# Optimization experiments

Hardware: AMD Instinct MI355X
Metric: run time of the kernel (lower is better)

Reference implementation:

```python
import jax, jax.numpy as jnp
import numpy as np

N_NODES = 100000
N_EDGES = 1200000
D = 64
N_LAYERS = 3


def setup_inputs() -> dict:
    key = jax.random.key(0)
    k0, k1, k2, k3, k4 = jax.random.split(key, 5)
    x = jax.random.normal(k0, (N_NODES, D), dtype=jnp.float32)
    edge_index = jax.random.randint(k1, (2, N_EDGES), 0, N_NODES, dtype=jnp.int32)
    edge_weight = jax.random.uniform(k2, (N_EDGES,), dtype=jnp.float32)
    # stacked per-layer params: 3 layers of 64->64
    self_kernels = jax.random.normal(k3, (N_LAYERS, D, D), dtype=jnp.float32) * 0.1
    neighbor_kernels = jax.random.normal(k4, (N_LAYERS, D, D), dtype=jnp.float32) * 0.1
    biases = jnp.zeros((N_LAYERS, D), dtype=jnp.float32)
    return {"x": x, "edge_index": edge_index, "edge_weight": edge_weight,
            "self_kernels": self_kernels, "neighbor_kernels": neighbor_kernels,
            "biases": biases}


def _sage_layer(h, row, col, edge_weight, self_k, neigh_k, b):
    # gather source-node features per edge, weight them: [E, d]
    msg = h[col] * edge_weight[:, None]
    # sum-aggregate messages at target nodes: [N, d]
    agg = jax.ops.segment_sum(msg, row, num_segments=N_NODES)
    # concat=False -> self transform + neighbor transform added, then relu
    out = h @ self_k + agg @ neigh_k + b
    return jax.nn.relu(out)


def reference(x, edge_index, edge_weight, self_kernels, neighbor_kernels, biases):
    row, col = edge_index[0], edge_index[1]
    h = x
    for i in range(N_LAYERS):
        h = _sage_layer(h, row, col, edge_weight,
                        self_kernels[i], neighbor_kernels[i], biases[i])
    return h
```

## Files before the change

### kernel.cpp

```cpp
#include <hip/hip_runtime.h>

#define NN 100000
#define NE 1200000
#define DD 64
#define NTILES 3125
#define NBK 391
#define MLEN (NBK * 256)
#define EPB 4688
#define ECAP 768

typedef unsigned int uint32;
typedef unsigned char uint8;
typedef unsigned short ushort16;
typedef __attribute__((ext_vector_type(8))) short short8;
typedef __attribute__((ext_vector_type(16))) float f32x16;

__device__ __forceinline__ ushort16 f2bf(float x) {
    uint32 u = __float_as_uint(x);
    u += 0x7FFFu + ((u >> 16) & 1u);
    return (ushort16)(u >> 16);
}
__device__ __forceinline__ float bflo(uint32 u) { return __uint_as_float(u << 16); }
__device__ __forceinline__ float bfhi(uint32 u) { return __uint_as_float(u & 0xFFFF0000u); }
__device__ __forceinline__ uint32 pack2(float a, float b) {
    return (uint32)f2bf(a) | ((uint32)f2bf(b) << 16);
}

__device__ __forceinline__ void agg_lds(float* a, int ls, int le, uint32 flB,
                                        const uint2* __restrict__ esh,
                                        const char* __restrict__ ybase) {
    #pragma unroll 4
    for (int j = ls; j < le; j++) {
        uint2 ei = esh[j];
        float w = __uint_as_float(ei.y);
        uint4 yv = *(const uint4*)(ybase + (ei.x + flB));
        a[0] = fmaf(bflo(yv.x), w, a[0]);
        a[1] = fmaf(bfhi(yv.x), w, a[1]);
        a[2] = fmaf(bflo(yv.y), w, a[2]);
        a[3] = fmaf(bfhi(yv.y), w, a[3]);
        a[4] = fmaf(bflo(yv.z), w, a[4]);
        a[5] = fmaf(bfhi(yv.z), w, a[5]);
        a[6] = fmaf(bflo(yv.w), w, a[6]);
        a[7] = fmaf(bfhi(yv.w), w, a[7]);
    }
}

__device__ __forceinline__ void agg_glob(float* a, int s, int e, uint32 flB,
                                         const uint32* __restrict__ edges,
                                         const char* __restrict__ ybase) {
    for (int j = s; j < e; j++) {
        uint32 ed = edges[j];
        float w = (float)(ed & 32767u) * (1.0f / 32767.0f);
        uint4 yv = *(const uint4*)(ybase + (((ed >> 15) << 7) + flB));
        a[0] = fmaf(bflo(yv.x), w, a[0]);
        a[1] = fmaf(bfhi(yv.x), w, a[1]);
        a[2] = fmaf(bflo(yv.y), w, a[2]);
        a[3] = fmaf(bfhi(yv.y), w, a[3]);
        a[4] = fmaf(bflo(yv.z), w, a[4]);
        a[5] = fmaf(bfhi(yv.z), w, a[5]);
        a[6] = fmaf(bflo(yv.w), w, a[6]);
        a[7] = fmaf(bfhi(yv.w), w, a[7]);
    }
}


__global__ __launch_bounds__(512)
void k_init(const int* __restrict__ row, int* __restrict__ M,
            const float* __restrict__ selfk, const float* __restrict__ neighk,
            short8* __restrict__ wpack, const float* __restrict__ x,
            ushort16* __restrict__ hs, ushort16* __restrict__ y,
            const float* __restrict__ biases) {
    if (blockIdx.x >= 262) {
        int lane  = threadIdx.x & 63;
        int wave  = threadIdx.x >> 6;
        int wid   = (blockIdx.x - 262) * 8 + wave;
        int mrow  = lane & 31;
        int khalf = lane >> 5;
        int t     = wid & 1;

        short8 Wf[2][4];
        #pragma unroll
        for (int g = 0; g < 2; g++) {
            const float* W = g ? neighk : selfk;
            #pragma unroll
            for (int s = 0; s < 4; s++) {
                int k0 = s * 16 + khalf * 8;
                short8 v;
                #pragma unroll
                for (int j = 0; j < 8; j++)
                    v[j] = (short)f2bf(W[(k0 + j) * 64 + t * 32 + mrow]);
                Wf[g][s] = v;
            }
        }
        float bval = biases[t * 32 + mrow];

        for (int tile = wid >> 1; tile < NTILES; tile += 1564) {
            int n0 = tile * 32;
            const float* hf = x + (n0 + mrow) * 64 + khalf * 8;
            short8 A[4];
            #pragma unroll
            for (int s = 0; s < 4; s++) {
                short8 a;
                #pragma unroll
                for (int j = 0; j < 8; j++) a[j] = (short)f2bf(hf[s * 16 + j]);
                A[s] = a;
            }

            f32x16 acc0, acc1;
            #pragma unroll
            for (int r = 0; r < 16; r++) { acc0[r] = 0.f; acc1[r] = 0.f; }

            #pragma unroll
            for (int s = 0; s < 4; s++) {
                acc0 = __builtin_amdgcn_mfma_f32_32x32x16_bf16(A[s], Wf[0][s], acc0, 0, 0, 0);
                acc1 = __builtin_amdgcn_mfma_f32_32x32x16_bf16(A[s], Wf[1][s], acc1, 0, 0, 0);
            }

            int colbase = t * 32 + mrow;
            #pragma unroll
            for (int r = 0; r < 16; r++) {
                int rw = (r & 3) + 8 * (r >> 2) + 4 * khalf;
                int nn = n0 + rw;
                hs[nn * DD + colbase] = f2bf(acc0[r] + bval);
                y [nn * DD + colbase] = f2bf(acc1[r]);
            }
        }
        return;
    }
    if (blockIdx.x >= 256) {
        int tid = (blockIdx.x - 256) * 512 + threadIdx.x;
        if (tid < 3 * 16 * 64) {
            int lane  = tid & 63;
            int frag  = (tid >> 6) & 15;
            int layer = tid >> 10;
            int g = frag >> 3;
            int t = (frag >> 2) & 1;
            int s = frag & 3;
            const float* W = (g ? neighk : selfk) + layer * 4096;
            int n = t * 32 + (lane & 31);
            int k0 = s * 16 + (lane >> 5) * 8;
            short8 v;
            #pragma unroll
            for (int j = 0; j < 8; j++) v[j] = (short)f2bf(W[(k0 + j) * 64 + n]);
            wpack[tid] = v;
        }
        return;
    }
    __shared__ int bins[NBK];
    for (int i = threadIdx.x; i < NBK; i += 512) bins[i] = 0;
    __syncthreads();
    int start = blockIdx.x * EPB;
    int end = min(start + EPB, NE);
    for (int e = start + (int)threadIdx.x; e < end; e += 512)
        atomicAdd(&bins[row[e] >> 8], 1);
    __syncthreads();
    for (int i = threadIdx.x; i < NBK; i += 512)
        M[i * 256 + blockIdx.x] = bins[i];
}


__global__ void k_scan1(const int* __restrict__ in, int* __restrict__ outx,
                        int* __restrict__ partials) {
    __shared__ int tmp[256];
    int t = threadIdx.x;
    int i = blockIdx.x * 256 + t;
    int v = (i < MLEN) ? in[i] : 0;
    tmp[t] = v;
    __syncthreads();
    #pragma unroll
    for (int off = 1; off < 256; off <<= 1) {
        int add = (t >= off) ? tmp[t - off] : 0;
        __syncthreads();
        tmp[t] += add;
        __syncthreads();
    }
    if (i < MLEN) outx[i] = tmp[t] - v;
    if (t == 255) partials[blockIdx.x] = tmp[255];
}

__global__ __launch_bounds__(512)
void k_bscatter(const int* __restrict__ row, const int* __restrict__ col,
                const float* __restrict__ ew, const int* __restrict__ Mscan,
                const int* __restrict__ partials, int* __restrict__ partials2,
                uint32* __restrict__ colw, uint8* __restrict__ rowlo) {
    __shared__ int tmp[512];
    __shared__ int cur[NBK];
    int t = threadIdx.x;
    int v = (t < NBK) ? partials[t] : 0;
    tmp[t] = v;
    __syncthreads();
    #pragma unroll
    for (int off = 1; off < 512; off <<= 1) {
        int add = (t >= off) ? tmp[t - off] : 0;
        __syncthreads();
        tmp[t] += add;
        __syncthreads();
    }
    if (t < NBK) {
        int excl = tmp[t] - v;
        cur[t] = Mscan[t * 256 + blockIdx.x] + excl;
        if (blockIdx.x == 0) partials2[t] = excl;
    }
    __syncthreads();
    int start = blockIdx.x * EPB;
    int end = min(start + EPB, NE);
    for (int e = start + (int)threadIdx.x; e < end; e += 512) {
        int r = row[e];
        int wq = (int)(ew[e] * 32767.0f + 0.5f);
        wq = (wq > 32767) ? 32767 : wq;
        int p = atomicAdd(&cur[r >> 8], 1);
        colw[p]  = ((uint32)col[e] << 15) | (uint32)wq;
        rowlo[p] = (uint8)(r & 255);
    }
}

__global__ __launch_bounds__(256)
void k_build(const int* __restrict__ Mscan, const int* __restrict__ partials2,
             const uint32* __restrict__ colw, const uint8* __restrict__ rowlo,
             uint32* __restrict__ edges, int* __restrict__ offsets) {
    __shared__ int bins[256];
    __shared__ int tmp[256];
    __shared__ int cur[256];
    int b = blockIdx.x;
    int t = threadIdx.x;
    int bstart = Mscan[b * 256] + partials2[b];
    int bend   = (b == NBK - 1) ? NE : Mscan[(b + 1) * 256] + partials2[b + 1];
    bins[t] = 0;
    __syncthreads();
    for (int p = bstart + t; p < bend; p += 256)
        atomicAdd(&bins[rowlo[p]], 1);
    __syncthreads();
    int v = bins[t];
    tmp[t] = v;
    __syncthreads();
    #pragma unroll
    for (int off = 1; off < 256; off <<= 1) {
        int add = (t >= off) ? tmp[t - off] : 0;
        __syncthreads();
        tmp[t] += add;
        __syncthreads();
    }
    int base = bstart + (tmp[t] - v);
    cur[t] = base;
    int rowid = b * 256 + t;
    if (rowid < NN) offsets[rowid] = base;
    if (b == 0 && t == 0) offsets[NN] = NE;
    __syncthreads();
    for (int p = bstart + t; p < bend; p += 256) {
        uint32 cw = colw[p];
        int dst = atomicAdd(&cur[rowlo[p]], 1);
        edges[dst] = cw;
    }
}


__global__ __launch_bounds__(256)
void agg_gemm(const uint4* __restrict__ hs4, const uint4* __restrict__ y4,
              ushort16* __restrict__ hs_out, ushort16* __restrict__ y_out,
              const int* __restrict__ offsets, const uint32* __restrict__ edges,
              const short8* __restrict__ wpack, const float* __restrict__ bias) {
    __shared__ uint32 sh[32 * 36];
    __shared__ uint2 esh[ECAP];
    int lane = threadIdx.x & 63;
    int wave = threadIdx.x >> 6;
    int g  = lane >> 3;
    int fl = lane & 7;
    int n0 = blockIdx.x * 32;
    int lrow = wave * 8 + g;
    int n = n0 + lrow;

    int ebase = offsets[n0];
    int m = min(offsets[n0 + 32] - ebase, ECAP);
    for (int i = threadIdx.x; i < m; i += 256) {
        uint32 ed = edges[ebase + i];
        esh[i] = make_uint2((ed >> 15) << 7,
                            __float_as_uint((float)(ed & 32767u) * (1.0f / 32767.0f)));
    }
    int s = offsets[n];
    int e = offsets[n + 1];
    uint4 hv = hs4[n * 8 + fl];
    __syncthreads();

    float a[8] = {bflo(hv.x), bfhi(hv.x), bflo(hv.y), bfhi(hv.y),
                  bflo(hv.z), bfhi(hv.z), bflo(hv.w), bfhi(hv.w)};
    uint32 flB = (uint32)fl * 16u;
    const char* ybase = (const char*)y4;
    int ls = s - ebase, le = e - ebase;
    agg_lds(a, min(ls, ECAP), min(le, ECAP), flB, esh, ybase);
    if (le > ECAP)
        agg_glob(a, ebase + max(ls, ECAP), ebase + le, flB, edges, ybase);

    uint32* dstp = &sh[lrow * 36 + fl * 4];
    dstp[0] = pack2(fmaxf(a[0], 0.f), fmaxf(a[1], 0.f));
    dstp[1] = pack2(fmaxf(a[2], 0.f), fmaxf(a[3], 0.f));
    dstp[2] = pack2(fmaxf(a[4], 0.f), fmaxf(a[5], 0.f));
    dstp[3] = pack2(fmaxf(a[6], 0.f), fmaxf(a[7], 0.f));
    __syncthreads();

    int mrow  = lane & 31;
    int khalf = lane >> 5;
    int gsel  = wave >> 1;
    int t     = wave & 1;

    short8 Wf[4];
    #pragma unroll
    for (int ss = 0; ss < 4; ss++)
        Wf[ss] = wpack[(((gsel * 2 + t) * 4) + ss) * 64 + lane];

    short8 A[4];
    #pragma unroll
    for (int ss = 0; ss < 4; ss++)
        A[ss] = *(const short8*)&sh[mrow * 36 + ss * 8 + khalf * 4];

    f32x16 acc;
    #pragma unroll
    for (int r = 0; r < 16; r++) acc[r] = 0.f;
    #pragma unroll
    for (int ss = 0; ss < 4; ss++)
        acc = __builtin_amdgcn_mfma_f32_32x32x16_bf16(A[ss], Wf[ss], acc, 0, 0, 0);

    float bval = gsel ? 0.f : bias[t * 32 + mrow];
    ushort16* dst = gsel ? y_out : hs_out;
    int colbase = t * 32 + mrow;
    #pragma unroll
    for (int r = 0; r < 16; r++) {
        int rw = (r & 3) + 8 * (r >> 2) + 4 * khalf;
        dst[(n0 + rw) * DD + colbase] = f2bf(acc[r] + bval);
    }
}


__global__ __launch_bounds__(256)
void agg_final(const uint4* __restrict__ hs4, const uint4* __restrict__ y4,
               float4* __restrict__ out, const int* __restrict__ offsets,
               const uint32* __restrict__ edges) {
    __shared__ uint2 esh[ECAP];
    int lane = threadIdx.x & 63;
    int wave = threadIdx.x >> 6;
    int g  = lane >> 3;
    int fl = lane & 7;
    int n0 = blockIdx.x * 32;
    int n = n0 + wave * 8 + g;

    int ebase = offsets[n0];
    int m = min(offsets[n0 + 32] - ebase, ECAP);
    for (int i = threadIdx.x; i < m; i += 256) {
        uint32 ed = edges[ebase + i];
        esh[i] = make_uint2((ed >> 15) << 7,
                            __float_as_uint((float)(ed & 32767u) * (1.0f / 32767.0f)));
    }
    int s = offsets[n];
    int e = offsets[n + 1];
    uint4 hv = hs4[n * 8 + fl];
    __syncthreads();

    float a[8] = {bflo(hv.x), bfhi(hv.x), bflo(hv.y), bfhi(hv.y),
                  bflo(hv.z), bfhi(hv.z), bflo(hv.w), bfhi(hv.w)};
    uint32 flB = (uint32)fl * 16u;
    const char* ybase = (const char*)y4;
    int ls = s - ebase, le = e - ebase;
    agg_lds(a, min(ls, ECAP), min(le, ECAP), flB, esh, ybase);
    if (le > ECAP)
        agg_glob(a, ebase + max(ls, ECAP), ebase + le, flB, edges, ybase);

    out[n * 16 + fl * 2]     = make_float4(fmaxf(a[0], 0.f), fmaxf(a[1], 0.f),
                                           fmaxf(a[2], 0.f), fmaxf(a[3], 0.f));
    out[n * 16 + fl * 2 + 1] = make_float4(fmaxf(a[4], 0.f), fmaxf(a[5], 0.f),
                                           fmaxf(a[6], 0.f), fmaxf(a[7], 0.f));
}


extern "C" void kernel_launch(void* const* d_in, const int* in_sizes, int n_in,
                              void* d_out, int out_size, void* d_ws, size_t ws_size,
                              hipStream_t stream) {
    const float* x      = (const float*)d_in[0];
    const int*   ei     = (const int*)d_in[1];
    const float* ew     = (const float*)d_in[2];
    const float* selfk  = (const float*)d_in[3];
    const float* neighk = (const float*)d_in[4];
    const float* biases = (const float*)d_in[5];
    float* out = (float*)d_out;

    char* w = (char*)d_ws;
    ushort16* hsA   = (ushort16*)w; w += (size_t)NN * DD * sizeof(ushort16);
    ushort16* yA    = (ushort16*)w; w += (size_t)NN * DD * sizeof(ushort16);
    ushort16* hsB   = (ushort16*)w; w += (size_t)NN * DD * sizeof(ushort16);
    ushort16* yB    = (ushort16*)w; w += (size_t)NN * DD * sizeof(ushort16);
    uint32* edges   = (uint32*)w;   w += (size_t)NE * sizeof(uint32);
    uint32* colwB   = (uint32*)w;   w += (size_t)NE * sizeof(uint32);
    uint8*  rowlo   = (uint8*)w;    w += (size_t)NE * sizeof(uint8);
    w = (char*)(((size_t)w + 255) & ~(size_t)255);
    int*    M       = (int*)w;      w += (size_t)MLEN * sizeof(int);
    int*    Mscan   = (int*)w;      w += (size_t)MLEN * sizeof(int);
    int*    offsets = (int*)w;      w += (size_t)(NN + 1) * sizeof(int);
    int*    partials= (int*)w;      w += 512 * sizeof(int);
    int*    partials2=(int*)w;      w += 512 * sizeof(int);
    short8* wpack   = (short8*)w;   w += (size_t)3 * 16 * 64 * sizeof(short8);

    const int* row = ei;
    const int* col = ei + NE;

    k_init    <<<653, 512, 0, stream>>>(row, M, selfk, neighk, wpack,
                                        x, hsA, yA, biases);
    k_scan1   <<<NBK, 256, 0, stream>>>(M, Mscan, partials);
    k_bscatter<<<256, 512, 0, stream>>>(row, col, ew, Mscan, partials, partials2,
                                        colwB, rowlo);
    k_build   <<<NBK, 256, 0, stream>>>(Mscan, partials2, colwB, rowlo, edges, offsets);

    agg_gemm <<<NTILES, 256, 0, stream>>>((const uint4*)hsA, (const uint4*)yA,
                                          hsB, yB, offsets, edges,
                                          wpack + 1024, biases + 64);
    agg_gemm <<<NTILES, 256, 0, stream>>>((const uint4*)hsB, (const uint4*)yB,
                                          hsA, yA, offsets, edges,
                                          wpack + 2048, biases + 128);
    agg_final<<<NTILES, 256, 0, stream>>>((const uint4*)hsA, (const uint4*)yA,
                                          (float4*)out, offsets, edges);
}
```

Measured before the change: 231.9 us.

## Balance edge aggregation across rows with LDS atomics and segment partitioning

Replaces per-row CSR aggregation, where each 8-lane group walked its own node's edge list, with an edge-balanced scheme. The block's edges are split evenly across the 32 row groups, each edge is tagged with its local row via binary search, and per-run partial sums are flushed to an LDS fp32 accumulator with atomics. The aim is to remove load imbalance from skewed node degrees, at the cost of extra LDS traffic and atomics. It also raises the LDS edge cache capacity and vectorizes the fp32 input loads in the init GEMM.

```diff
diff --git a/kernel.cpp b/kernel.cpp
--- a/kernel.cpp
+++ b/kernel.cpp
@@ -7,7 +7,7 @@
 #define NBK 391
 #define MLEN (NBK * 256)
 #define EPB 4688
-#define ECAP 768
+#define ECAP 1024
 
 typedef unsigned int uint32;
 typedef unsigned char uint8;
@@ -24,43 +24,6 @@
 __device__ __forceinline__ float bfhi(uint32 u) { return __uint_as_float(u & 0xFFFF0000u); }
 __device__ __forceinline__ uint32 pack2(float a, float b) {
     return (uint32)f2bf(a) | ((uint32)f2bf(b) << 16);
-}
-
-__device__ __forceinline__ void agg_lds(float* a, int ls, int le, uint32 flB,
-                                        const uint2* __restrict__ esh,
-                                        const char* __restrict__ ybase) {
-    #pragma unroll 4
-    for (int j = ls; j < le; j++) {
-        uint2 ei = esh[j];
-        float w = __uint_as_float(ei.y);
-        uint4 yv = *(const uint4*)(ybase + (ei.x + flB));
-        a[0] = fmaf(bflo(yv.x), w, a[0]);
-        a[1] = fmaf(bfhi(yv.x), w, a[1]);
-        a[2] = fmaf(bflo(yv.y), w, a[2]);
-        a[3] = fmaf(bfhi(yv.y), w, a[3]);
-        a[4] = fmaf(bflo(yv.z), w, a[4]);
-        a[5] = fmaf(bfhi(yv.z), w, a[5]);
-        a[6] = fmaf(bflo(yv.w), w, a[6]);
-        a[7] = fmaf(bfhi(yv.w), w, a[7]);
-    }
-}
-
-__device__ __forceinline__ void agg_glob(float* a, int s, int e, uint32 flB,
-                                         const uint32* __restrict__ edges,
-                                         const char* __restrict__ ybase) {
-    for (int j = s; j < e; j++) {
-        uint32 ed = edges[j];
-        float w = (float)(ed & 32767u) * (1.0f / 32767.0f);
-        uint4 yv = *(const uint4*)(ybase + (((ed >> 15) << 7) + flB));
-        a[0] = fmaf(bflo(yv.x), w, a[0]);
-        a[1] = fmaf(bfhi(yv.x), w, a[1]);
-        a[2] = fmaf(bflo(yv.y), w, a[2]);
-        a[3] = fmaf(bfhi(yv.y), w, a[3]);
-        a[4] = fmaf(bflo(yv.z), w, a[4]);
-        a[5] = fmaf(bfhi(yv.z), w, a[5]);
-        a[6] = fmaf(bflo(yv.w), w, a[6]);
-        a[7] = fmaf(bfhi(yv.w), w, a[7]);
-    }
 }
 
 
@@ -96,13 +59,18 @@
 
         for (int tile = wid >> 1; tile < NTILES; tile += 1564) {
             int n0 = tile * 32;
-            const float* hf = x + (n0 + mrow) * 64 + khalf * 8;
+            const float4* hf4 = (const float4*)(x + (size_t)(n0 + mrow) * 64)
+                                + khalf * 2;
             short8 A[4];
             #pragma unroll
             for (int s = 0; s < 4; s++) {
+                float4 q0 = hf4[s * 4];
+                float4 q1 = hf4[s * 4 + 1];
                 short8 a;
-                #pragma unroll
-                for (int j = 0; j < 8; j++) a[j] = (short)f2bf(hf[s * 16 + j]);
+                a[0] = (short)f2bf(q0.x); a[1] = (short)f2bf(q0.y);
+                a[2] = (short)f2bf(q0.z); a[3] = (short)f2bf(q0.w);
+                a[4] = (short)f2bf(q1.x); a[5] = (short)f2bf(q1.y);
+                a[6] = (short)f2bf(q1.z); a[7] = (short)f2bf(q1.w);
                 A[s] = a;
             }
 
@@ -259,42 +227,114 @@
               ushort16* __restrict__ hs_out, ushort16* __restrict__ y_out,
               const int* __restrict__ offsets, const uint32* __restrict__ edges,
               const short8* __restrict__ wpack, const float* __restrict__ bias) {
-    __shared__ uint32 sh[32 * 36];
-    __shared__ uint2 esh[ECAP];
-    int lane = threadIdx.x & 63;
-    int wave = threadIdx.x >> 6;
+    __shared__ __align__(16) uint32 ubuf[ECAP * 2];
+    __shared__ float sacc[32 * 65];
+    __shared__ int loff[33];
+    uint2* esh = (uint2*)ubuf;
+    int tid  = threadIdx.x;
+    int lane = tid & 63;
+    int wave = tid >> 6;
     int g  = lane >> 3;
     int fl = lane & 7;
     int n0 = blockIdx.x * 32;
     int lrow = wave * 8 + g;
     int n = n0 + lrow;
 
-    int ebase = offsets[n0];
-    int m = min(offsets[n0 + 32] - ebase, ECAP);
-    for (int i = threadIdx.x; i < m; i += 256) {
+    if (tid < 33) loff[tid] = offsets[n0 + tid];
+    uint4 hv = hs4[n * 8 + fl];
+    {
+        float* ap = &sacc[lrow * 65 + fl * 8];
+        ap[0] = bflo(hv.x); ap[1] = bfhi(hv.x);
+        ap[2] = bflo(hv.y); ap[3] = bfhi(hv.y);
+        ap[4] = bflo(hv.z); ap[5] = bfhi(hv.z);
+        ap[6] = bflo(hv.w); ap[7] = bfhi(hv.w);
+    }
+    __syncthreads();
+
+    int ebase = loff[0];
+    int m  = loff[32] - ebase;
+    int mm = min(m, ECAP);
+    for (int i = tid; i < mm; i += 256) {
         uint32 ed = edges[ebase + i];
-        esh[i] = make_uint2((ed >> 15) << 7,
+        int gi = ebase + i;
+        int lo = 0, hi = 32;
+        #pragma unroll
+        for (int st = 0; st < 5; st++) {
+            int mid = (lo + hi) >> 1;
+            if (loff[mid] <= gi) lo = mid; else hi = mid;
+        }
+        esh[i] = make_uint2(((ed >> 15) << 7) | (uint32)lo,
                             __float_as_uint((float)(ed & 32767u) * (1.0f / 32767.0f)));
     }
-    int s = offsets[n];
-    int e = offsets[n + 1];
-    uint4 hv = hs4[n * 8 + fl];
-    __syncthreads();
-
-    float a[8] = {bflo(hv.x), bfhi(hv.x), bflo(hv.y), bfhi(hv.y),
-                  bflo(hv.z), bfhi(hv.z), bflo(hv.w), bfhi(hv.w)};
+    __syncthreads();
+
     uint32 flB = (uint32)fl * 16u;
     const char* ybase = (const char*)y4;
-    int ls = s - ebase, le = e - ebase;
-    agg_lds(a, min(ls, ECAP), min(le, ECAP), flB, esh, ybase);
-    if (le > ECAP)
-        agg_glob(a, ebase + max(ls, ECAP), ebase + le, flB, edges, ybase);
-
-    uint32* dstp = &sh[lrow * 36 + fl * 4];
-    dstp[0] = pack2(fmaxf(a[0], 0.f), fmaxf(a[1], 0.f));
-    dstp[1] = pack2(fmaxf(a[2], 0.f), fmaxf(a[3], 0.f));
-    dstp[2] = pack2(fmaxf(a[4], 0.f), fmaxf(a[5], 0.f));
-    dstp[3] = pack2(fmaxf(a[6], 0.f), fmaxf(a[7], 0.f));
+    int chunk = (mm + 31) >> 5;
+    int j0 = lrow * chunk;
+    int j1 = min(j0 + chunk, mm);
+    float r0=0.f,r1=0.f,r2=0.f,r3=0.f,r4=0.f,r5=0.f,r6=0.f,r7=0.f;
+    int curr = -1;
+    #pragma unroll 2
+    for (int j = j0; j < j1; j++) {
+        uint2 e = esh[j];
+        int r = (int)(e.x & 31u);
+        float w = __uint_as_float(e.y);
+        uint4 yv = *(const uint4*)(ybase + ((e.x & 0xFFFFFF80u) + flB));
+        if (r != curr) {
+            if (curr >= 0) {
+                float* p = &sacc[curr * 65 + fl * 8];
+                atomicAdd(p+0, r0); atomicAdd(p+1, r1);
+                atomicAdd(p+2, r2); atomicAdd(p+3, r3);
+                atomicAdd(p+4, r4); atomicAdd(p+5, r5);
+                atomicAdd(p+6, r6); atomicAdd(p+7, r7);
+            }
+            r0=r1=r2=r3=r4=r5=r6=r7=0.f;
+            curr = r;
+        }
+        r0 = fmaf(bflo(yv.x), w, r0);
+        r1 = fmaf(bfhi(yv.x), w, r1);
+        r2 = fmaf(bflo(yv.y), w, r2);
+        r3 = fmaf(bfhi(yv.y), w, r3);
+        r4 = fmaf(bflo(yv.z), w, r4);
+        r5 = fmaf(bfhi(yv.z), w, r5);
+        r6 = fmaf(bflo(yv.w), w, r6);
+        r7 = fmaf(bfhi(yv.w), w, r7);
+    }
+    if (curr >= 0) {
+        float* p = &sacc[curr * 65 + fl * 8];
+        atomicAdd(p+0, r0); atomicAdd(p+1, r1);
+        atomicAdd(p+2, r2); atomicAdd(p+3, r3);
+        atomicAdd(p+4, r4); atomicAdd(p+5, r5);
+        atomicAdd(p+6, r6); atomicAdd(p+7, r7);
+    }
+    for (int i = ECAP + lrow; i < m; i += 32) {
+        uint32 ed = edges[ebase + i];
+        int gi = ebase + i;
+        int lo = 0, hi = 32;
+        for (int st = 0; st < 5; st++) {
+            int mid = (lo + hi) >> 1;
+            if (loff[mid] <= gi) lo = mid; else hi = mid;
+        }
+        float w = (float)(ed & 32767u) * (1.0f / 32767.0f);
+        uint4 yv = *(const uint4*)(ybase + (((ed >> 15) << 7) + flB));
+        float* p = &sacc[lo * 65 + fl * 8];
+        atomicAdd(p+0, bflo(yv.x)*w); atomicAdd(p+1, bfhi(yv.x)*w);
+        atomicAdd(p+2, bflo(yv.y)*w); atomicAdd(p+3, bfhi(yv.y)*w);
+        atomicAdd(p+4, bflo(yv.z)*w); atomicAdd(p+5, bfhi(yv.z)*w);
+        atomicAdd(p+6, bflo(yv.w)*w); atomicAdd(p+7, bfhi(yv.w)*w);
+    }
+    __syncthreads();
+
+    uint32* sh = ubuf;
+    {
+        float* q = &sacc[lrow * 65 + fl * 8];
+        uint32* dstp = &sh[lrow * 36 + fl * 4];
+        dstp[0] = pack2(fmaxf(q[0], 0.f), fmaxf(q[1], 0.f));
+        dstp[1] = pack2(fmaxf(q[2], 0.f), fmaxf(q[3], 0.f));
+        dstp[2] = pack2(fmaxf(q[4], 0.f), fmaxf(q[5], 0.f));
+        dstp[3] = pack2(fmaxf(q[6], 0.f), fmaxf(q[7], 0.f));
+    }
     __syncthreads();
 
     int mrow  = lane & 31;
@@ -334,39 +374,110 @@
 void agg_final(const uint4* __restrict__ hs4, const uint4* __restrict__ y4,
                float4* __restrict__ out, const int* __restrict__ offsets,
                const uint32* __restrict__ edges) {
-    __shared__ uint2 esh[ECAP];
-    int lane = threadIdx.x & 63;
-    int wave = threadIdx.x >> 6;
+    __shared__ __align__(16) uint32 ubuf[ECAP * 2];
+    __shared__ float sacc[32 * 65];
+    __shared__ int loff[33];
+    uint2* esh = (uint2*)ubuf;
+    int tid  = threadIdx.x;
+    int lane = tid & 63;
+    int wave = tid >> 6;
     int g  = lane >> 3;
     int fl = lane & 7;
     int n0 = blockIdx.x * 32;
-    int n = n0 + wave * 8 + g;
-
-    int ebase = offsets[n0];
-    int m = min(offsets[n0 + 32] - ebase, ECAP);
-    for (int i = threadIdx.x; i < m; i += 256) {
+    int lrow = wave * 8 + g;
+    int n = n0 + lrow;
+
+    if (tid < 33) loff[tid] = offsets[n0 + tid];
+    uint4 hv = hs4[n * 8 + fl];
+    {
+        float* ap = &sacc[lrow * 65 + fl * 8];
+        ap[0] = bflo(hv.x); ap[1] = bfhi(hv.x);
+        ap[2] = bflo(hv.y); ap[3] = bfhi(hv.y);
+        ap[4] = bflo(hv.z); ap[5] = bfhi(hv.z);
+        ap[6] = bflo(hv.w); ap[7] = bfhi(hv.w);
+    }
+    __syncthreads();
+
+    int ebase = loff[0];
+    int m  = loff[32] - ebase;
+    int mm = min(m, ECAP);
+    for (int i = tid; i < mm; i += 256) {
         uint32 ed = edges[ebase + i];
-        esh[i] = make_uint2((ed >> 15) << 7,
+        int gi = ebase + i;
+        int lo = 0, hi = 32;
+        #pragma unroll
+        for (int st = 0; st < 5; st++) {
+            int mid = (lo + hi) >> 1;
+            if (loff[mid] <= gi) lo = mid; else hi = mid;
+        }
+        esh[i] = make_uint2(((ed >> 15) << 7) | (uint32)lo,
                             __float_as_uint((float)(ed & 32767u) * (1.0f / 32767.0f)));
     }
-    int s = offsets[n];
-    int e = offsets[n + 1];
-    uint4 hv = hs4[n * 8 + fl];
-    __syncthreads();
-
-    float a[8] = {bflo(hv.x), bfhi(hv.x), bflo(hv.y), bfhi(hv.y),
-                  bflo(hv.z), bfhi(hv.z), bflo(hv.w), bfhi(hv.w)};
+    __syncthreads();
+
     uint32 flB = (uint32)fl * 16u;
     const char* ybase = (const char*)y4;
-    int ls = s - ebase, le = e - ebase;
-    agg_lds(a, min(ls, ECAP), min(le, ECAP), flB, esh, ybase);
-    if (le > ECAP)
-        agg_glob(a, ebase + max(ls, ECAP), ebase + le, flB, edges, ybase);
-
-    out[n * 16 + fl * 2]     = make_float4(fmaxf(a[0], 0.f), fmaxf(a[1], 0.f),
-                                           fmaxf(a[2], 0.f), fmaxf(a[3], 0.f));
-    out[n * 16 + fl * 2 + 1] = make_float4(fmaxf(a[4], 0.f), fmaxf(a[5], 0.f),
-                                           fmaxf(a[6], 0.f), fmaxf(a[7], 0.f));
+    int chunk = (mm + 31) >> 5;
+    int j0 = lrow * chunk;
+    int j1 = min(j0 + chunk, mm);
+    float r0=0.f,r1=0.f,r2=0.f,r3=0.f,r4=0.f,r5=0.f,r6=0.f,r7=0.f;
+    int curr = -1;
+    #pragma unroll 2
+    for (int j = j0; j < j1; j++) {
+        uint2 e = esh[j];
+        int r = (int)(e.x & 31u);
+        float w = __uint_as_float(e.y);
+        uint4 yv = *(const uint4*)(ybase + ((e.x & 0xFFFFFF80u) + flB));
+        if (r != curr) {
+            if (curr >= 0) {
+                float* p = &sacc[curr * 65 + fl * 8];
+                atomicAdd(p+0, r0); atomicAdd(p+1, r1);
+                atomicAdd(p+2, r2); atomicAdd(p+3, r3);
+                atomicAdd(p+4, r4); atomicAdd(p+5, r5);
+                atomicAdd(p+6, r6); atomicAdd(p+7, r7);
+            }
+            r0=r1=r2=r3=r4=r5=r6=r7=0.f;
+            curr = r;
+        }
+        r0 = fmaf(bflo(yv.x), w, r0);
+        r1 = fmaf(bfhi(yv.x), w, r1);
+        r2 = fmaf(bflo(yv.y), w, r2);
+        r3 = fmaf(bfhi(yv.y), w, r3);
+        r4 = fmaf(bflo(yv.z), w, r4);
+        r5 = fmaf(bfhi(yv.z), w, r5);
+        r6 = fmaf(bflo(yv.w), w, r6);
+        r7 = fmaf(bfhi(yv.w), w, r7);
+    }
+    if (curr >= 0) {
+        float* p = &sacc[curr * 65 + fl * 8];
+        atomicAdd(p+0, r0); atomicAdd(p+1, r1);
+        atomicAdd(p+2, r2); atomicAdd(p+3, r3);
+        atomicAdd(p+4, r4); atomicAdd(p+5, r5);
+        atomicAdd(p+6, r6); atomicAdd(p+7, r7);
+    }
+    for (int i = ECAP + lrow; i < m; i += 32) {
+        uint32 ed = edges[ebase + i];
+        int gi = ebase + i;
+        int lo = 0, hi = 32;
+        for (int st = 0; st < 5; st++) {
+            int mid = (lo + hi) >> 1;
+            if (loff[mid] <= gi) lo = mid; else hi = mid;
+        }
+        float w = (float)(ed & 32767u) * (1.0f / 32767.0f);
+        uint4 yv = *(const uint4*)(ybase + (((ed >> 15) << 7) + flB));
+        float* p = &sacc[lo * 65 + fl * 8];
+        atomicAdd(p+0, bflo(yv.x)*w); atomicAdd(p+1, bfhi(yv.x)*w);
+        atomicAdd(p+2, bflo(yv.y)*w); atomicAdd(p+3, bfhi(yv.y)*w);
+        atomicAdd(p+4, bflo(yv.z)*w); atomicAdd(p+5, bfhi(yv.z)*w);
+        atomicAdd(p+6, bflo(yv.w)*w); atomicAdd(p+7, bfhi(yv.w)*w);
+    }
+    __syncthreads();
+
+    float* q = &sacc[lrow * 65 + fl * 8];
+    out[n * 16 + fl * 2]     = make_float4(fmaxf(q[0], 0.f), fmaxf(q[1], 0.f),
+                                           fmaxf(q[2], 0.f), fmaxf(q[3], 0.f));
+    out[n * 16 + fl * 2 + 1] = make_float4(fmaxf(q[4], 0.f), fmaxf(q[5], 0.f),
+                                           fmaxf(q[6], 0.f), fmaxf(q[7], 0.f));
 }
 
 
```

After: 353.0 us. 1.52x slower.
